# Performance work log

Measured on AMD Instinct MI355X. Metric: run time of the kernel, lower is better.

## Reference

```python
import jax, jax.numpy as jnp
import numpy as np

QW, KW = 64, 128          # atom query / key window sizes
PAD = (KW - QW) // 2      # halo on each side of the key window
DEPTH, HEADS = 3, 4

def ln(x):
    m = jnp.mean(x, -1, keepdims=True)
    v = jnp.var(x, -1, keepdims=True)
    return (x - m) * jax.lax.rsqrt(v + 1e-5)

def q_windows(x):
    # x: (B, N, ...) -> (B, n, QW, ...); N assumed multiple of QW
    B, N = x.shape[0], x.shape[1]
    n = N // QW
    return x.reshape((B, n, QW) + x.shape[2:])

def k_windows(x):
    # x: (B, N, ...) -> (B, n, KW, ...) sliding key windows with zero halo padding
    B, N = x.shape[0], x.shape[1]
    n = N // QW
    pad_cfg = [(0, 0), (PAD, n * QW + PAD - N)] + [(0, 0)] * (x.ndim - 2)
    xp = jnp.pad(x, pad_cfg)
    idx = jnp.arange(n)[:, None] * QW + jnp.arange(KW)[None, :]
    return xp[:, idx]


def setup_inputs() -> dict:
    key = jax.random.key(0)
    ks = jax.random.split(key, 24)
    B, N, DS, DP, DT, NT = 2, 8192, 128, 16, 384, 1024
    w = lambda k, shp: (jax.random.normal(k, shp, jnp.float32) / np.sqrt(shp[-2])).astype(jnp.float32)
    inp = {
        'ref_pos': jax.random.normal(ks[0], (B, N, 3), jnp.float32),
        'ref_charge': jax.random.normal(ks[1], (B, N, 1), jnp.float32),
        'ref_mask': jnp.ones((B, N, 1), jnp.float32),
        'ref_element': jax.random.uniform(ks[2], (B, N, 128), jnp.float32),
        'ref_atom_name_chars': jax.random.uniform(ks[3], (B, N, 256), jnp.float32),
        'W_single': w(ks[4], (389, DS)),
        'W_pair': w(ks[5], (5, DP)),
        'W_outer': w(ks[6], (DS, 2 * DP)),
        'Wp_ff1': w(ks[7], (DP, 4 * DP)),
        'Wp_ff2': w(ks[8], (4 * DP, DP)),
        'Wq': w(ks[9], (DEPTH, DS, DS)),
        'Wk': w(ks[10], (DEPTH, DS, DS)),
        'Wv': w(ks[11], (DEPTH, DS, DS)),
        'Wo': w(ks[12], (DEPTH, DS, DS)),
        'Wb': w(ks[13], (DP, HEADS)),
        'Wff1': w(ks[14], (DEPTH, DS, 4 * DS)),
        'Wff2': w(ks[15], (DEPTH, 4 * DS, DS)),
        'W_out': w(ks[16], (DS, DT)),
        'ref_space_uid': jnp.sort(jax.random.randint(ks[17], (B, N), 0, NT), axis=-1),
        'atom_to_token_idx': jnp.sort(jax.random.randint(ks[18], (B, N), 0, NT), axis=-1),
        'n_tokens': NT,
    }
    return inp


def reference(ref_pos, ref_charge, ref_mask, ref_element, ref_atom_name_chars,
              W_single, W_pair, W_outer, Wp_ff1, Wp_ff2,
              Wq, Wk, Wv, Wo, Wb, Wff1, Wff2, W_out,
              ref_space_uid, atom_to_token_idx, n_tokens):
    B, N, _ = ref_pos.shape
    n = N // QW
    feats = jnp.concatenate([ref_pos, ref_charge, ref_mask, ref_element, ref_atom_name_chars], -1)
    s = feats @ W_single                                    # (B,N,DS) atom single repr

    # windowed pairwise geometric features
    pos_i, pos_j = q_windows(ref_pos), k_windows(ref_pos)   # (B,n,QW,3), (B,n,KW,3)
    uid_i, uid_j = q_windows(ref_space_uid), k_windows(ref_space_uid)
    dij = pos_i[:, :, :, None, :] - pos_j[:, :, None, :, :]  # (B,n,QW,KW,3)
    inv = 1.0 / (1.0 + jnp.sum(dij * dij, -1, keepdims=True))
    bij = (uid_i[:, :, :, None] == uid_j[:, :, None, :])
    pf = jnp.concatenate([dij, inv, bij[..., None].astype(dij.dtype)], -1)  # (...,5)
    pair = (pf @ W_pair) * bij[..., None].astype(dij.dtype)  # (B,n,QW,KW,DP)

    # pairwise outer-add from relu(single): Linear(DS->2*DP) split into i/j halves
    p = jax.nn.relu(s) @ W_outer
    DP = pair.shape[-1]
    pi, pj = p[..., :DP], p[..., DP:]
    pair = pair + q_windows(pi)[:, :, :, None, :] + k_windows(pj)[:, :, None, :, :]
    pair = pair + jax.nn.relu(ln(pair) @ Wp_ff1) @ Wp_ff2    # pair FF (residual)
    bias = jnp.einsum('bnqkc,ch->bnhqk', pair, Wb)           # attn pair bias

    # key validity mask for the halo-padded positions
    kidx = jnp.arange(n)[:, None] * QW + jnp.arange(KW)[None, :] - PAD
    kmask = jnp.where((kidx >= 0) & (kidx < N), 0.0, -1e9).astype(s.dtype)  # (n,KW)

    dh = s.shape[-1] // HEADS
    x = s
    for l in range(DEPTH):
        h = ln(x)
        q = q_windows(h @ Wq[l]).reshape(B, n, QW, HEADS, dh)
        k = k_windows(h @ Wk[l]).reshape(B, n, KW, HEADS, dh)
        v = k_windows(h @ Wv[l]).reshape(B, n, KW, HEADS, dh)
        logits = jnp.einsum('bnqhd,bnkhd->bnhqk', q, k) / np.sqrt(dh)
        logits = logits + bias + kmask[None, :, None, None, :]
        a = jax.nn.softmax(logits, -1)
        o = jnp.einsum('bnhqk,bnkhd->bnqhd', a, v).reshape(B, N, -1) @ Wo[l]
        x = x + o
        x = x + jax.nn.relu(ln(x) @ Wff1[l]) @ Wff2[l]

    tok = jax.nn.relu(x @ W_out)                             # (B,N,DT)

    def seg_mean(src, idx_):
        ssum = jax.ops.segment_sum(src, idx_, num_segments=n_tokens)
        cnt = jax.ops.segment_sum(jnp.ones((src.shape[0],), src.dtype), idx_, num_segments=n_tokens)
        return ssum / jnp.clip(cnt, 1.0)[:, None]

    return jax.vmap(seg_mean)(tok, atom_to_token_idx)        # (B, n_tokens, DT)
```

## Files before the change

### kernel.cpp

```cpp
#include <hip/hip_runtime.h>
#include <hip/hip_bf16.h>

#define QW 64
#define KW 128
#define PADW 32
#define DEPTH 3
#define HEADS 4
#define B_ 2
#define N_ 8192
#define DS 128
#define DP 16
#define DT 384
#define NT 1024
#define NWIN (N_ / QW)
#define DH (DS / HEADS)

typedef unsigned short u16;
typedef __attribute__((ext_vector_type(8))) short short8;
typedef __attribute__((ext_vector_type(4))) float f32x4v;
typedef __attribute__((ext_vector_type(4))) unsigned short us4;

__device__ __forceinline__ u16 f2b(float x) {
    union { float f; unsigned u; } v; v.f = x;
    unsigned r = v.u + 0x7fffu + ((v.u >> 16) & 1u);
    return (u16)(r >> 16);
}
__device__ __forceinline__ float b2f(u16 h) {
    union { unsigned u; float f; } v; v.u = ((unsigned)h) << 16; return v.f;
}
__device__ __forceinline__ unsigned f2b2(float a, float b) {
    __hip_bfloat162 h = __float22bfloat162_rn(make_float2(a, b));
    union { __hip_bfloat162 h; unsigned u; } c; c.h = h; return c.u;
}
__device__ __forceinline__ us4 pack4(float a, float b, float c, float d) {
    union { us4 v; unsigned u[2]; } o;
    o.u[0] = f2b2(a, b);
    o.u[1] = f2b2(c, d);
    return o.v;
}

__global__ __launch_bounds__(256) void convw_kernel(
    const float* __restrict__ Wq, const float* __restrict__ Wk,
    const float* __restrict__ Wv, const float* __restrict__ Wo,
    const float* __restrict__ Wff1, const float* __restrict__ Wff2,
    const float* __restrict__ Wout, const float* __restrict__ Wpff1,
    const float* __restrict__ Wpff2, const float* __restrict__ Wb,
    const float* __restrict__ Wsingle, const float* __restrict__ Wouter,
    u16* __restrict__ qkvT, u16* __restrict__ woT, u16* __restrict__ ff1T,
    u16* __restrict__ ff2T, u16* __restrict__ woutT,
    u16* __restrict__ w1T32, u16* __restrict__ wcatT,
    u16* __restrict__ wsT, u16* __restrict__ woutrT)
{
    int idx = blockIdx.x * 256 + threadIdx.x;
    if (idx < 3 * 384 * 128) {
        int l = idx / (384 * 128), r = idx % (384 * 128);
        int n = r / 128, k = r % 128;
        const float* W = (n < 128) ? Wq : (n < 256) ? Wk : Wv;
        qkvT[idx] = f2b(W[(size_t)l * 16384 + k * 128 + (n & 127)]);
    }
    if (idx < 3 * 128 * 128) {
        int l = idx / 16384, r = idx % 16384;
        int n = r / 128, k = r % 128;
        woT[idx] = f2b(Wo[(size_t)l * 16384 + k * 128 + n]);
    }
    if (idx < 3 * 512 * 128) {
        int l = idx / 65536, r = idx % 65536;
        int n = r / 128, k = r % 128;
        ff1T[idx] = f2b(Wff1[(size_t)l * 65536 + k * 512 + n]);
    }
    if (idx < 3 * 128 * 512) {
        int l = idx / 65536, r = idx % 65536;
        int n = r / 512, k = r % 512;
        ff2T[idx] = f2b(Wff2[(size_t)l * 65536 + k * 128 + n]);
    }
    if (idx < 384 * 128) {
        int n = idx / 128, k = idx % 128;
        woutT[idx] = f2b(Wout[(size_t)k * 384 + n]);
    }
    if (idx < 64 * 32) {
        int n = idx >> 5, k = idx & 31;
        w1T32[idx] = (k < 16) ? f2b(Wpff1[k * 64 + n]) : (u16)0;
    }
    if (idx < 16 * 96) {
        int h = idx / 96, k = idx % 96;
        float s = 0.f;
        if (h < 4) {
            if (k < 16) s = Wb[k * 4 + h];
            else if (k < 80) {
                int j = k - 16;
                for (int c = 0; c < 16; ++c) s += Wpff2[j * 16 + c] * Wb[c * 4 + h];
            }
        }
        wcatT[idx] = f2b(s);
    }
    if (idx < 128 * 416) {
        int n = idx / 416, k = idx % 416;
        float v = 0.f;
        if (k < 128)       v = Wsingle[(5 + k) * 128 + n];
        else if (k < 384)  v = Wsingle[(133 + k - 128) * 128 + n];
        else if (k < 387)  v = Wsingle[(k - 384) * 128 + n];
        else if (k == 387) v = Wsingle[3 * 128 + n];
        else if (k == 388) v = Wsingle[4 * 128 + n];
        wsT[idx] = f2b(v);
    }
    if (idx < 32 * 128) {
        int n = idx >> 7, k = idx & 127;
        woutrT[idx] = f2b(Wouter[k * 32 + n]);
    }
}

__global__ __launch_bounds__(256) void embed_gemm(
    const float* __restrict__ pos, const float* __restrict__ charge,
    const float* __restrict__ mask, const float* __restrict__ elem,
    const float* __restrict__ chars, const u16* __restrict__ wsT,
    const u16* __restrict__ woutrT,
    float* __restrict__ X, u16* __restrict__ LNb, float* __restrict__ P)
{
    __shared__ __align__(16) u16 As[64 * 424];
    __shared__ float redS[64][4];
    int tid = threadIdx.x;
    int row0 = blockIdx.x * 64;

    #pragma unroll
    for (int it = 0; it < 8; ++it) {
        int idx = tid + it * 256;
        int r = idx >> 5, c4 = idx & 31;
        f32x4v v = *(const f32x4v*)(elem + (size_t)(row0 + r) * 128 + c4 * 4);
        *(us4*)&As[r * 424 + c4 * 4] = pack4(v[0], v[1], v[2], v[3]);
    }
    #pragma unroll
    for (int it = 0; it < 16; ++it) {
        int idx = tid + it * 256;
        int r = idx >> 6, c4 = idx & 63;
        f32x4v v = *(const f32x4v*)(chars + (size_t)(row0 + r) * 256 + c4 * 4);
        *(us4*)&As[r * 424 + 128 + c4 * 4] = pack4(v[0], v[1], v[2], v[3]);
    }
    if (tid < 64) {
        int g = row0 + tid;
        As[tid * 424 + 384] = f2b(pos[g * 3]);
        As[tid * 424 + 385] = f2b(pos[g * 3 + 1]);
        As[tid * 424 + 386] = f2b(pos[g * 3 + 2]);
        As[tid * 424 + 387] = f2b(charge[g]);
        As[tid * 424 + 388] = f2b(mask[g]);
        for (int c = 389; c < 416; ++c) As[tid * 424 + c] = 0;
    }
    __syncthreads();

    int wv = tid >> 6, lane = tid & 63, quad = lane >> 4, l16 = lane & 15;
    int wm = (wv & 1) * 32, wn = (wv >> 1) * 64;
    f32x4v acc[2][4];
    #pragma unroll
    for (int i = 0; i < 2; ++i)
        #pragma unroll
        for (int j = 0; j < 4; ++j) acc[i][j] = (f32x4v){0.f, 0.f, 0.f, 0.f};

    #pragma unroll
    for (int kk = 0; kk < 13; ++kk) {
        short8 a0 = *(short8*)&As[(wm + l16) * 424 + kk * 32 + quad * 8];
        short8 a1 = *(short8*)&As[(wm + 16 + l16) * 424 + kk * 32 + quad * 8];
        #pragma unroll
        for (int nt = 0; nt < 4; ++nt) {
            short8 bw = *(const short8*)&wsT[(size_t)(wn + nt * 16 + l16) * 416 +
                                             kk * 32 + quad * 8];
            acc[0][nt] = __builtin_amdgcn_mfma_f32_16x16x32_bf16(a0, bw, acc[0][nt], 0, 0, 0);
            acc[1][nt] = __builtin_amdgcn_mfma_f32_16x16x32_bf16(a1, bw, acc[1][nt], 0, 0, 0);
        }
    }
    __syncthreads();

    #pragma unroll
    for (int mt = 0; mt < 2; ++mt) {
        #pragma unroll
        for (int r = 0; r < 4; ++r) {
            int lrow = wm + mt * 16 + quad * 4 + r;
            int row = row0 + lrow;
            float s = 0.f, ss = 0.f;
            #pragma unroll
            for (int nt = 0; nt < 4; ++nt) {
                float v = acc[mt][nt][r];
                int col = wn + nt * 16 + l16;
                X[(size_t)row * DS + col] = v;
                As[lrow * 136 + col] = f2b(fmaxf(v, 0.f));
                s += v; ss += v * v;
            }
            #pragma unroll
            for (int o = 1; o < 16; o <<= 1) {
                s  += __shfl_xor(s, o);
                ss += __shfl_xor(ss, o);
            }
            if (l16 == 0) {
                redS[lrow][(wv >> 1) * 2]     = s;
                redS[lrow][(wv >> 1) * 2 + 1] = ss;
            }
        }
    }
    __syncthreads();

    #pragma unroll
    for (int mt = 0; mt < 2; ++mt)
        #pragma unroll
        for (int r = 0; r < 4; ++r) {
            int lrow = wm + mt * 16 + quad * 4 + r;
            int row = row0 + lrow;
            f32x4v rv = *(f32x4v*)&redS[lrow][0];
            float s = rv[0] + rv[2], ss = rv[1] + rv[3];
            float m = s * (1.f / 128.f);
            float var = ss * (1.f / 128.f) - m * m;
            float rs = rsqrtf(var + 1e-5f);
            #pragma unroll
            for (int nt = 0; nt < 4; ++nt) {
                int col = wn + nt * 16 + l16;
                LNb[(size_t)row * DS + col] = f2b((acc[mt][nt][r] - m) * rs);
            }
        }

    {
        f32x4v pacc[2];
        pacc[0] = (f32x4v){0.f, 0.f, 0.f, 0.f};
        pacc[1] = (f32x4v){0.f, 0.f, 0.f, 0.f};
        #pragma unroll
        for (int ks = 0; ks < 4; ++ks) {
            short8 a = *(short8*)&As[(wv * 16 + l16) * 136 + ks * 32 + quad * 8];
            #pragma unroll
            for (int nt = 0; nt < 2; ++nt) {
                short8 bw = *(const short8*)&woutrT[(size_t)(nt * 16 + l16) * 128 +
                                                    ks * 32 + quad * 8];
                pacc[nt] = __builtin_amdgcn_mfma_f32_16x16x32_bf16(a, bw, pacc[nt], 0, 0, 0);
            }
        }
        #pragma unroll
        for (int nt = 0; nt < 2; ++nt)
            #pragma unroll
            for (int r = 0; r < 4; ++r) {
                int row = row0 + wv * 16 + quad * 4 + r;
                P[(size_t)row * 32 + nt * 16 + l16] = pacc[nt][r];
            }
    }
}

__global__ __launch_bounds__(256) void bias_kernel(
    const float* __restrict__ pos, const int* __restrict__ uid,
    const float* __restrict__ P, const float* __restrict__ Wpair,
    const u16* __restrict__ w1T32, const u16* __restrict__ wcatT,
    u16* __restrict__ BIASb)
{
    __shared__ __align__(16) float posjS[128][4];
    __shared__ __align__(16) u16 lpS[4][16 * 24];
    __shared__ __align__(16) u16 A2S[4][16 * 104];

    int tid = threadIdx.x;
    int b  = blockIdx.x >> 11;
    int w  = (blockIdx.x >> 4) & 127;
    int qg = blockIdx.x & 15;

    if (tid < 128) {
        int r = tid;
        int jk = w * QW + r - PADW;
        bool valid = (jk >= 0) && (jk < N_);
        int gk = b * N_ + jk;
        float x = 0.f, y = 0.f, zz = 0.f; int u = 0;
        if (valid) { x = pos[gk * 3]; y = pos[gk * 3 + 1]; zz = pos[gk * 3 + 2]; u = uid[gk]; }
        posjS[r][0] = x; posjS[r][1] = y; posjS[r][2] = zz;
        ((int*)posjS[r])[3] = u;
    }

    int wv = tid >> 6, lane = tid & 63, quad = lane >> 4, l16 = lane & 15;
    int cl = lane >> 2, cg = lane & 3;
    int q = qg * 4 + wv;
    int gq = b * N_ + w * QW + q;

    float xi = pos[gq * 3], yi = pos[gq * 3 + 1], zi = pos[gq * 3 + 2];
    int ui = uid[gq];
    f32x4v pi4 = *(const f32x4v*)(P + (size_t)gq * 32 + cg * 4);
    f32x4v wp[5];
    #pragma unroll
    for (int f = 0; f < 5; ++f)
        wp[f] = *(const f32x4v*)(Wpair + f * 16 + cg * 4);
    short8 w1f[4], wcat[3];
    #pragma unroll
    for (int nt = 0; nt < 4; ++nt)
        w1f[nt] = *(const short8*)&w1T32[(nt * 16 + l16) * 32 + quad * 8];
    #pragma unroll
    for (int ks = 0; ks < 3; ++ks)
        wcat[ks] = *(const short8*)&wcatT[l16 * 96 + ks * 32 + quad * 8];

    f32x4v pjv[8];
    #pragma unroll
    for (int t = 0; t < 8; ++t) {
        int jk = w * QW + t * 16 + cl - PADW;
        bool valid = (jk >= 0) && (jk < N_);
        int gk = b * N_ + jk;
        f32x4v v = (f32x4v){0.f, 0.f, 0.f, 0.f};
        if (valid) v = *(const f32x4v*)(P + (size_t)gk * 32 + 16 + cg * 4);
        pjv[t] = v;
    }

    *(us4*)&A2S[wv][l16 * 104 + 80 + quad * 4] = (us4){0, 0, 0, 0};
    __syncthreads();

    size_t bbase = ((size_t)(b * NWIN + w) * HEADS) * (QW * KW);
    const short8 zero8 = (short8){0, 0, 0, 0, 0, 0, 0, 0};

    for (int t = 0; t < 8; ++t) {
        int kk1 = t * 16 + cl;
        float xj = posjS[kk1][0], yj = posjS[kk1][1], zj = posjS[kk1][2];
        int uj = ((int*)posjS[kk1])[3];
        float dx = xi - xj, dy = yi - yj, dz = zi - zj;
        float inv = 1.f / (1.f + dx * dx + dy * dy + dz * dz);
        float bf = (ui == uj) ? 1.f : 0.f;
        float pr[4];
        #pragma unroll
        for (int j = 0; j < 4; ++j) {
            float s = fmaf(dx, wp[0][j], fmaf(dy, wp[1][j],
                      fmaf(dz, wp[2][j], fmaf(inv, wp[3][j], wp[4][j]))));
            pr[j] = fmaf(bf, s, pi4[j] + pjv[t][j]);
        }
        float sum = pr[0] + pr[1] + pr[2] + pr[3];
        sum += __shfl_xor(sum, 1); sum += __shfl_xor(sum, 2);
        float m = sum * (1.f / 16.f);
        float d0 = pr[0] - m, d1 = pr[1] - m, d2 = pr[2] - m, d3 = pr[3] - m;
        float vs = d0 * d0 + d1 * d1 + d2 * d2 + d3 * d3;
        vs += __shfl_xor(vs, 1); vs += __shfl_xor(vs, 2);
        float rstd = rsqrtf(vs * (1.f / 16.f) + 1e-5f);
        *(us4*)&lpS[wv][cl * 24 + cg * 4] =
            pack4(d0 * rstd, d1 * rstd, d2 * rstd, d3 * rstd);
        *(us4*)&A2S[wv][cl * 104 + cg * 4] = pack4(pr[0], pr[1], pr[2], pr[3]);

        short8 blp = zero8;
        if (quad < 2) blp = *(short8*)&lpS[wv][l16 * 24 + quad * 8];
        #pragma unroll
        for (int nt = 0; nt < 4; ++nt) {
            f32x4v z4 = (f32x4v){0.f, 0.f, 0.f, 0.f};
            z4 = __builtin_amdgcn_mfma_f32_16x16x32_bf16(w1f[nt], blp, z4, 0, 0, 0);
            *(us4*)&A2S[wv][l16 * 104 + 16 + nt * 16 + quad * 4] =
                pack4(fmaxf(z4[0], 0.f), fmaxf(z4[1], 0.f),
                      fmaxf(z4[2], 0.f), fmaxf(z4[3], 0.f));
        }
        f32x4v acc = (f32x4v){0.f, 0.f, 0.f, 0.f};
        #pragma unroll
        for (int ks = 0; ks < 3; ++ks) {
            short8 a2 = *(short8*)&A2S[wv][l16 * 104 + ks * 32 + quad * 8];
            acc = __builtin_amdgcn_mfma_f32_16x16x32_bf16(a2, wcat[ks], acc, 0, 0, 0);
        }
        if (l16 < 4) {
            *(us4*)&BIASb[bbase + (size_t)l16 * (QW * KW) + q * KW +
                          t * 16 + quad * 4] = pack4(acc[0], acc[1], acc[2], acc[3]);
        }
    }
}

template <bool RELU>
__global__ __launch_bounds__(256) void gemm_bf(
    const u16* __restrict__ A, const u16* __restrict__ WT,
    u16* __restrict__ OutB, int N)
{
    __shared__ __align__(16) u16 As[64 * 136];
    int tid = threadIdx.x;
    int row0 = blockIdx.x * 64, n0 = blockIdx.y * 128;

    #pragma unroll
    for (int it = 0; it < 4; ++it) {
        int idx = tid + it * 256;
        int r = idx >> 4, c8 = idx & 15;
        *(short8*)&As[r * 136 + c8 * 8] =
            *(const short8*)&A[(size_t)(row0 + r) * 128 + c8 * 8];
    }
    __syncthreads();

    int wv = tid >> 6, lane = tid & 63, quad = lane >> 4, l16 = lane & 15;
    int wm = (wv & 1) * 32, wn = (wv >> 1) * 64;
    f32x4v acc[2][4];
    #pragma unroll
    for (int i = 0; i < 2; ++i)
        #pragma unroll
        for (int j = 0; j < 4; ++j) acc[i][j] = (f32x4v){0.f, 0.f, 0.f, 0.f};

    #pragma unroll
    for (int kk = 0; kk < 4; ++kk) {
        short8 a0 = *(short8*)&As[(wm + l16) * 136 + kk * 32 + quad * 8];
        short8 a1 = *(short8*)&As[(wm + 16 + l16) * 136 + kk * 32 + quad * 8];
        #pragma unroll
        for (int nt = 0; nt < 4; ++nt) {
            short8 bw = *(const short8*)&WT[(size_t)(n0 + wn + nt * 16 + l16) * 128 +
                                            kk * 32 + quad * 8];
            acc[0][nt] = __builtin_amdgcn_mfma_f32_16x16x32_bf16(a0, bw, acc[0][nt], 0, 0, 0);
            acc[1][nt] = __builtin_amdgcn_mfma_f32_16x16x32_bf16(a1, bw, acc[1][nt], 0, 0, 0);
        }
    }
    #pragma unroll
    for (int mt = 0; mt < 2; ++mt)
        #pragma unroll
        for (int nt = 0; nt < 4; ++nt)
            #pragma unroll
            for (int r = 0; r < 4; ++r) {
                int row = row0 + wm + mt * 16 + quad * 4 + r;
                int col = n0 + wn + nt * 16 + l16;
                float v = acc[mt][nt][r];
                if (RELU) v = fmaxf(v, 0.f);
                OutB[(size_t)row * N + col] = f2b(v);
            }
}

__global__ __launch_bounds__(256) void wo_ff_fused(
    const u16* __restrict__ Ob, const u16* __restrict__ woT,
    const u16* __restrict__ w1T, const u16* __restrict__ w2T,
    float* __restrict__ X, u16* __restrict__ LNb)
{
    __shared__ __align__(16) u16 As[32 * 136];
    __shared__ __align__(16) u16 Hs[32 * 520];
    __shared__ float redS[32][4];
    int tid = threadIdx.x;
    int row0 = blockIdx.x * 32;
    int wv = tid >> 6, lane = tid & 63, quad = lane >> 4, l16 = lane & 15;
    int wm = (wv & 1) * 16, wn = (wv >> 1) * 64;

    #pragma unroll
    for (int it = 0; it < 2; ++it) {
        int idx = tid + it * 256;
        int r = idx >> 4, c8 = idx & 15;
        *(short8*)&As[r * 136 + c8 * 8] =
            *(const short8*)&Ob[(size_t)(row0 + r) * 128 + c8 * 8];
    }
    __syncthreads();

    f32x4v acc[4];
    #pragma unroll
    for (int j = 0; j < 4; ++j) acc[j] = (f32x4v){0.f, 0.f, 0.f, 0.f};
    #pragma unroll
    for (int ks = 0; ks < 4; ++ks) {
        short8 a = *(short8*)&As[(wm + l16) * 136 + ks * 32 + quad * 8];
        #pragma unroll
        for (int nt = 0; nt < 4; ++nt) {
            short8 b = *(const short8*)&woT[(size_t)(wn + nt * 16 + l16) * 128 +
                                            ks * 32 + quad * 8];
            acc[nt] = __builtin_amdgcn_mfma_f32_16x16x32_bf16(a, b, acc[nt], 0, 0, 0);
        }
    }
    __syncthreads();

    #pragma unroll
    for (int r = 0; r < 4; ++r) {
        int lrow = wm + quad * 4 + r;
        int row = row0 + lrow;
        float s = 0.f, ss = 0.f;
        #pragma unroll
        for (int nt = 0; nt < 4; ++nt) {
            int col = wn + nt * 16 + l16;
            float v = acc[nt][r] + X[(size_t)row * DS + col];
            acc[nt][r] = v;
            s += v; ss += v * v;
        }
        #pragma unroll
        for (int o2 = 1; o2 < 16; o2 <<= 1) {
            s  += __shfl_xor(s, o2);
            ss += __shfl_xor(ss, o2);
        }
        if (l16 == 0) {
            redS[lrow][(wv >> 1) * 2]     = s;
            redS[lrow][(wv >> 1) * 2 + 1] = ss;
        }
    }
    __syncthreads();

    #pragma unroll
    for (int r = 0; r < 4; ++r) {
        int lrow = wm + quad * 4 + r;
        f32x4v rv = *(f32x4v*)&redS[lrow][0];
        float s = rv[0] + rv[2], ss = rv[1] + rv[3];
        float m = s * (1.f / 128.f);
        float var = ss * (1.f / 128.f) - m * m;
        float rs = rsqrtf(var + 1e-5f);
        #pragma unroll
        for (int nt = 0; nt < 4; ++nt) {
            int col = wn + nt * 16 + l16;
            As[lrow * 136 + col] = f2b((acc[nt][r] - m) * rs);
        }
    }
    __syncthreads();

    {
        short8 brow[2][4];
        #pragma unroll
        for (int nt = 0; nt < 2; ++nt)
            #pragma unroll
            for (int ks = 0; ks < 4; ++ks)
                brow[nt][ks] = *(short8*)&As[(nt * 16 + l16) * 136 + ks * 32 + quad * 8];
        #pragma unroll
        for (int mt = 0; mt < 8; ++mt) {
            int j0 = wv * 128 + mt * 16;
            f32x4v c0 = (f32x4v){0.f, 0.f, 0.f, 0.f};
            f32x4v c1 = (f32x4v){0.f, 0.f, 0.f, 0.f};
            #pragma unroll
            for (int ks = 0; ks < 4; ++ks) {
                short8 aw = *(const short8*)&w1T[(size_t)(j0 + l16) * 128 +
                                                 ks * 32 + quad * 8];
                c0 = __builtin_amdgcn_mfma_f32_16x16x32_bf16(aw, brow[0][ks], c0, 0, 0, 0);
                c1 = __builtin_amdgcn_mfma_f32_16x16x32_bf16(aw, brow[1][ks], c1, 0, 0, 0);
            }
            *(us4*)&Hs[l16 * 520 + j0 + quad * 4] =
                pack4(fmaxf(c0[0], 0.f), fmaxf(c0[1], 0.f),
                      fmaxf(c0[2], 0.f), fmaxf(c0[3], 0.f));
            *(us4*)&Hs[(16 + l16) * 520 + j0 + quad * 4] =
                pack4(fmaxf(c1[0], 0.f), fmaxf(c1[1], 0.f),
                      fmaxf(c1[2], 0.f), fmaxf(c1[3], 0.f));
        }
    }
    __syncthreads();

    f32x4v acc2[4];
    #pragma unroll
    for (int j = 0; j < 4; ++j) acc2[j] = (f32x4v){0.f, 0.f, 0.f, 0.f};
    #pragma unroll
    for (int ks = 0; ks < 16; ++ks) {
        short8 a = *(short8*)&Hs[(wm + l16) * 520 + ks * 32 + quad * 8];
        #pragma unroll
        for (int nt = 0; nt < 4; ++nt) {
            short8 b = *(const short8*)&w2T[(size_t)(wn + nt * 16 + l16) * 512 +
                                            ks * 32 + quad * 8];
            acc2[nt] = __builtin_amdgcn_mfma_f32_16x16x32_bf16(a, b, acc2[nt], 0, 0, 0);
        }
    }

    #pragma unroll
    for (int r = 0; r < 4; ++r) {
        int lrow = wm + quad * 4 + r;
        int row = row0 + lrow;
        float s = 0.f, ss = 0.f;
        #pragma unroll
        for (int nt = 0; nt < 4; ++nt) {
            int col = wn + nt * 16 + l16;
            float v = acc2[nt][r] + acc[nt][r];
            acc2[nt][r] = v;
            X[(size_t)row * DS + col] = v;
            s += v; ss += v * v;
        }
        #pragma unroll
        for (int o2 = 1; o2 < 16; o2 <<= 1) {
            s  += __shfl_xor(s, o2);
            ss += __shfl_xor(ss, o2);
        }
        if (l16 == 0) {
            redS[lrow][(wv >> 1) * 2]     = s;
            redS[lrow][(wv >> 1) * 2 + 1] = ss;
        }
    }
    __syncthreads();

    #pragma unroll
    for (int r = 0; r < 4; ++r) {
        int lrow = wm + quad * 4 + r;
        int row = row0 + lrow;
        f32x4v rv = *(f32x4v*)&redS[lrow][0];
        float s = rv[0] + rv[2], ss = rv[1] + rv[3];
        float m = s * (1.f / 128.f);
        float var = ss * (1.f / 128.f) - m * m;
        float rs = rsqrtf(var + 1e-5f);
        #pragma unroll
        for (int nt = 0; nt < 4; ++nt) {
            int col = wn + nt * 16 + l16;
            LNb[(size_t)row * DS + col] = f2b((acc2[nt][r] - m) * rs);
        }
    }
}

__global__ __launch_bounds__(256) void gemm_fin(
    const float* __restrict__ A, const u16* __restrict__ WT,
    u16* __restrict__ OutB, int K, int N)
{
    __shared__ __align__(16) u16 As[64 * 88];
    const int row0 = blockIdx.x * 64, n0 = blockIdx.y * 128;
    const int tid = threadIdx.x;
    const int w = tid >> 6, lane = tid & 63, quad = lane >> 4, l16 = lane & 15;
    const int wm = (w & 1) * 32, wn = (w >> 1) * 64;

    f32x4v acc[2][4];
    #pragma unroll
    for (int i = 0; i < 2; ++i)
        #pragma unroll
        for (int j = 0; j < 4; ++j) acc[i][j] = (f32x4v){0.f, 0.f, 0.f, 0.f};

    for (int k0 = 0; k0 < K; k0 += 64) {
        __syncthreads();
        #pragma unroll
        for (int it = 0; it < 4; ++it) {
            int idx = tid + it * 256;
            int r = idx >> 4, c = idx & 15;
            f32x4v v = *(const f32x4v*)(A + (size_t)(row0 + r) * K + k0 + c * 4);
            *(us4*)&As[r * 88 + c * 4] = pack4(v[0], v[1], v[2], v[3]);
        }
        __syncthreads();
        #pragma unroll
        for (int kk = 0; kk < 64; kk += 32) {
            short8 a0 = *(const short8*)&As[(wm + l16) * 88 + kk + quad * 8];
            short8 a1 = *(const short8*)&As[(wm + 16 + l16) * 88 + kk + quad * 8];
            #pragma unroll
            for (int nt = 0; nt < 4; ++nt) {
                short8 b = *(const short8*)&WT[(size_t)(n0 + wn + nt * 16 + l16) * K + k0 + kk + quad * 8];
                acc[0][nt] = __builtin_amdgcn_mfma_f32_16x16x32_bf16(a0, b, acc[0][nt], 0, 0, 0);
                acc[1][nt] = __builtin_amdgcn_mfma_f32_16x16x32_bf16(a1, b, acc[1][nt], 0, 0, 0);
            }
        }
    }
    #pragma unroll
    for (int mt = 0; mt < 2; ++mt)
        #pragma unroll
        for (int nt = 0; nt < 4; ++nt)
            #pragma unroll
            for (int r = 0; r < 4; ++r) {
                int row = row0 + wm + mt * 16 + quad * 4 + r;
                int col = n0 + wn + nt * 16 + l16;
                OutB[(size_t)row * N + col] = f2b(fmaxf(acc[mt][nt][r], 0.f));
            }
}

__global__ __launch_bounds__(256) void attn_kernel(
    const u16* __restrict__ QKV, const u16* __restrict__ BIASb,
    u16* __restrict__ O)
{
    __shared__ __align__(16) u16 sQ[64 * 40];
    __shared__ __align__(16) u16 sK[128 * 40];
    __shared__ __align__(16) u16 sVt[32 * 152];
    __shared__ __align__(16) u16 sP[64 * 136];
    __shared__ float pmax[4][64];
    __shared__ float psum[4][64];
    __shared__ float gfac[4][64];

    int tid = threadIdx.x;
    int h = blockIdx.x & 3, w = (blockIdx.x >> 2) & 127, b = blockIdx.x >> 9;
    size_t rowbase = (size_t)b * N_ + w * QW;
    size_t bbase = ((size_t)(b * NWIN + w) * HEADS + h) * (QW * KW);
    const short8 zero8 = (short8){0, 0, 0, 0, 0, 0, 0, 0};

    {
        int r = tid >> 2, d8 = (tid & 3) * 8;
        *(short8*)&sQ[r * 40 + d8] =
            *(const short8*)&QKV[(rowbase + r) * 384 + h * DH + d8];
    }
    #pragma unroll
    for (int i = 0; i < 2; ++i) {
        int idx = tid + i * 256;
        int r = idx >> 2, d8 = (idx & 3) * 8;
        int jk = w * QW + r - PADW;
        short8 v = zero8;
        if (jk >= 0 && jk < N_)
            v = *(const short8*)&QKV[((size_t)b * N_ + jk) * 384 + 128 + h * DH + d8];
        *(short8*)&sK[r * 40 + d8] = v;
    }
    {
        int kk = tid >> 1, d0 = (tid & 1) * 16;
        int jk = w * QW + kk - PADW;
        short8 v0 = zero8, v1 = zero8;
        if (jk >= 0 && jk < N_) {
            const u16* src = &QKV[((size_t)b * N_ + jk) * 384 + 256 + h * DH + d0];
            v0 = *(const short8*)src;
            v1 = *(const short8*)(src + 8);
        }
        #pragma unroll
        for (int j = 0; j < 8; ++j) {
            sVt[(d0 + j) * 152 + kk] = (u16)v0[j];
            sVt[(d0 + 8 + j) * 152 + kk] = (u16)v1[j];
        }
    }
    #pragma unroll
    for (int i = 0; i < 4; ++i) {
        int idx = tid + i * 256;
        int q = idx >> 4, c8 = idx & 15;
        *(short8*)&sP[q * 136 + c8 * 8] =
            *(const short8*)&BIASb[bbase + (size_t)q * KW + c8 * 8];
    }
    __syncthreads();

    int wv = tid >> 6, lane = tid & 63, quad = lane >> 4, l16 = lane & 15;
    const float scale = 0.17677669529663687f;

    short8 aq[4];
    #pragma unroll
    for (int mt = 0; mt < 4; ++mt)
        aq[mt] = *(short8*)&sQ[(mt * 16 + l16) * 40 + quad * 8];
    float e[2][4][4];
    #pragma unroll
    for (int ni = 0; ni < 2; ++ni) {
        int nt = wv * 2 + ni;
        short8 bk = *(short8*)&sK[(nt * 16 + l16) * 40 + quad * 8];
        int kk = nt * 16 + l16;
        int jk = w * QW + kk - PADW;
        float msk = (jk >= 0 && jk < N_) ? 0.f : -1e9f;
        #pragma unroll
        for (int mt = 0; mt < 4; ++mt) {
            f32x4v acc = (f32x4v){0.f, 0.f, 0.f, 0.f};
            acc = __builtin_amdgcn_mfma_f32_16x16x32_bf16(aq[mt], bk, acc, 0, 0, 0);
            #pragma unroll
            for (int r = 0; r < 4; ++r) {
                int q = mt * 16 + quad * 4 + r;
                e[ni][mt][r] = acc[r] * scale + b2f(sP[q * 136 + kk]) + msk;
            }
        }
    }

    #pragma unroll
    for (int mt = 0; mt < 4; ++mt)
        #pragma unroll
        for (int r = 0; r < 4; ++r) {
            float m = fmaxf(e[0][mt][r], e[1][mt][r]);
            m = fmaxf(m, __shfl_xor(m, 1));
            m = fmaxf(m, __shfl_xor(m, 2));
            m = fmaxf(m, __shfl_xor(m, 4));
            m = fmaxf(m, __shfl_xor(m, 8));
            float e0 = __expf(e[0][mt][r] - m);
            float e1 = __expf(e[1][mt][r] - m);
            e[0][mt][r] = e0; e[1][mt][r] = e1;
            float s = e0 + e1;
            s += __shfl_xor(s, 1);
            s += __shfl_xor(s, 2);
            s += __shfl_xor(s, 4);
            s += __shfl_xor(s, 8);
            if (l16 == 0) {
                int q = mt * 16 + quad * 4 + r;
                pmax[wv][q] = m;
                psum[wv][q] = s;
            }
        }
    __syncthreads();

    if (tid < 64) {
        float m0 = pmax[0][tid], m1 = pmax[1][tid], m2 = pmax[2][tid], m3 = pmax[3][tid];
        float M = fmaxf(fmaxf(m0, m1), fmaxf(m2, m3));
        float g0 = __expf(m0 - M), g1 = __expf(m1 - M),
              g2 = __expf(m2 - M), g3 = __expf(m3 - M);
        float T = psum[0][tid] * g0 + psum[1][tid] * g1 +
                  psum[2][tid] * g2 + psum[3][tid] * g3;
        float inv = 1.f / T;
        gfac[0][tid] = g0 * inv; gfac[1][tid] = g1 * inv;
        gfac[2][tid] = g2 * inv; gfac[3][tid] = g3 * inv;
    }
    __syncthreads();

    #pragma unroll
    for (int mt = 0; mt < 4; ++mt)
        #pragma unroll
        for (int r = 0; r < 4; ++r) {
            int q = mt * 16 + quad * 4 + r;
            float f = gfac[wv][q];
            #pragma unroll
            for (int ni = 0; ni < 2; ++ni) {
                int kk = (wv * 2 + ni) * 16 + l16;
                sP[q * 136 + kk] = f2b(e[ni][mt][r] * f);
            }
        }
    __syncthreads();

    {
        int mt = wv;
        short8 ap[4];
        #pragma unroll
        for (int ks = 0; ks < 4; ++ks)
            ap[ks] = *(short8*)&sP[(mt * 16 + l16) * 136 + ks * 32 + quad * 8];
        #pragma unroll
        for (int nt = 0; nt < 2; ++nt) {
            f32x4v acc = (f32x4v){0.f, 0.f, 0.f, 0.f};
            #pragma unroll
            for (int ks = 0; ks < 4; ++ks) {
                short8 bv = *(short8*)&sVt[(nt * 16 + l16) * 152 + ks * 32 + quad * 8];
                acc = __builtin_amdgcn_mfma_f32_16x16x32_bf16(ap[ks], bv, acc, 0, 0, 0);
            }
            int d = nt * 16 + l16;
            #pragma unroll
            for (int r = 0; r < 4; ++r) {
                int q = mt * 16 + quad * 4 + r;
                O[(rowbase + q) * DS + h * DH + d] = f2b(acc[r]);
            }
        }
    }
}

__global__ __launch_bounds__(128) void seg_kernel(
    const u16* __restrict__ TOKb, const int* __restrict__ idx,
    float* __restrict__ out)
{
    int t = blockIdx.x & (NT - 1);
    int b = blockIdx.x >> 10;
    const int* id = idx + (size_t)b * N_;

    int lo = 0, hi = N_;
    while (lo < hi) { int mid = (lo + hi) >> 1; if (id[mid] < t) lo = mid + 1; else hi = mid; }
    int start = lo;
    hi = N_;
    while (lo < hi) { int mid = (lo + hi) >> 1; if (id[mid] < t + 1) lo = mid + 1; else hi = mid; }
    int end = lo;

    float inv = 1.f / fmaxf((float)(end - start), 1.f);
    for (int c = threadIdx.x; c < DT; c += 128) {
        float s = 0.f;
        for (int r = start; r < end; ++r) s += b2f(TOKb[((size_t)b * N_ + r) * DT + c]);
        out[((size_t)b * NT + t) * DT + c] = s * inv;
    }
}

extern "C" void kernel_launch(void* const* d_in, const int* in_sizes, int n_in,
                              void* d_out, int out_size, void* d_ws, size_t ws_size,
                              hipStream_t stream)
{
    const float* ref_pos    = (const float*)d_in[0];
    const float* ref_charge = (const float*)d_in[1];
    const float* ref_mask   = (const float*)d_in[2];
    const float* ref_elem   = (const float*)d_in[3];
    const float* ref_chars  = (const float*)d_in[4];
    const float* W_single   = (const float*)d_in[5];
    const float* W_pair     = (const float*)d_in[6];
    const float* W_outer    = (const float*)d_in[7];
    const float* Wp_ff1     = (const float*)d_in[8];
    const float* Wp_ff2     = (const float*)d_in[9];
    const float* Wq         = (const float*)d_in[10];
    const float* Wk         = (const float*)d_in[11];
    const float* Wv         = (const float*)d_in[12];
    const float* Wo         = (const float*)d_in[13];
    const float* Wb         = (const float*)d_in[14];
    const float* Wff1       = (const float*)d_in[15];
    const float* Wff2       = (const float*)d_in[16];
    const float* W_out      = (const float*)d_in[17];
    const int*   uid        = (const int*)d_in[18];
    const int*   a2t        = (const int*)d_in[19];
    float* out = (float*)d_out;

    const size_t ROWS = (size_t)B_ * N_;
    float* ws = (float*)d_ws;
    float* X    = ws;
    float* P    = X + ROWS * DS;
    u16* QKVb   = (u16*)(P + ROWS * 32);
    u16* Ob     = QKVb + ROWS * 384;
    u16* FFb    = Ob + ROWS * DS;
    u16* BIASb  = FFb + ROWS * 512;
    u16* TOKb   = BIASb + (size_t)B_ * NWIN * HEADS * QW * KW;
    u16* LNb    = TOKb + ROWS * DT;
    u16* qkvT   = LNb + ROWS * DS;
    u16* woT    = qkvT + 3 * 384 * 128;
    u16* ff1T   = woT + 3 * 128 * 128;
    u16* ff2T   = ff1T + 3 * 512 * 128;
    u16* woutT  = ff2T + 3 * 128 * 512;
    u16* w1T32  = woutT + 384 * 128;
    u16* wcatT  = w1T32 + 64 * 32;
    u16* wsT    = wcatT + 16 * 96;
    u16* woutrT = wsT + 128 * 416;

    convw_kernel<<<768, 256, 0, stream>>>(Wq, Wk, Wv, Wo, Wff1, Wff2, W_out,
                                          Wp_ff1, Wp_ff2, Wb, W_single, W_outer,
                                          qkvT, woT, ff1T, ff2T, woutT,
                                          w1T32, wcatT, wsT, woutrT);
    embed_gemm<<<ROWS / 64, 256, 0, stream>>>(ref_pos, ref_charge, ref_mask,
                                              ref_elem, ref_chars, wsT, woutrT,
                                              X, LNb, P);
    bias_kernel<<<4096, 256, 0, stream>>>(ref_pos, uid, P, W_pair,
                                          w1T32, wcatT, BIASb);

    for (int l = 0; l < DEPTH; ++l) {
        gemm_bf<false><<<dim3(ROWS / 64, 3), 256, 0, stream>>>(
            LNb, qkvT + (size_t)l * 384 * 128, QKVb, 384);
        attn_kernel<<<B_ * NWIN * HEADS, 256, 0, stream>>>(QKVb, BIASb, Ob);
        wo_ff_fused<<<ROWS / 32, 256, 0, stream>>>(
            Ob, woT + (size_t)l * 128 * 128,
            ff1T + (size_t)l * 512 * 128, ff2T + (size_t)l * 128 * 512,
            X, LNb);
    }

    gemm_fin<<<dim3(ROWS / 64, 3), 256, 0, stream>>>(X, woutT, TOKb, DS, DT);
    seg_kernel<<<B_ * NT, 128, 0, stream>>>(TOKb, a2t, out);
}
```

Before: 405.6 us.

## Fuse QKV projection and output projection into preceding kernels' epilogues

The QKV projection GEMM moves into the epilogue of embed_gemm (layer 0) and wo_ff_fused (layers 1..2). The LayerNorm output stays in shared memory instead of round-tripping through global LNb. The final W_out GEMM with ReLU is likewise fused into the last wo_ff_fused, which removes four separate GEMM launches and the LNb/X reloads. In exchange, each fused block now reads all three 128-column weight chunks, and wo_ff_fused does a serial 32x384 GEMM per block, which lengthens those kernels.

New measurement: 405.1 us. About the same (-0.1%).

```diff
diff --git a/kernel.cpp b/kernel.cpp
--- a/kernel.cpp
+++ b/kernel.cpp
@@ -113,11 +113,12 @@
     const float* __restrict__ pos, const float* __restrict__ charge,
     const float* __restrict__ mask, const float* __restrict__ elem,
     const float* __restrict__ chars, const u16* __restrict__ wsT,
-    const u16* __restrict__ woutrT,
-    float* __restrict__ X, u16* __restrict__ LNb, float* __restrict__ P)
+    const u16* __restrict__ woutrT, const u16* __restrict__ qkv0T,
+    float* __restrict__ X, float* __restrict__ P, u16* __restrict__ QKVb)
 {
     __shared__ __align__(16) u16 As[64 * 424];
     __shared__ float redS[64][4];
+    const int LNOFF = 64 * 136;
     int tid = threadIdx.x;
     int row0 = blockIdx.x * 64;
 
@@ -201,7 +202,6 @@
         #pragma unroll
         for (int r = 0; r < 4; ++r) {
             int lrow = wm + mt * 16 + quad * 4 + r;
-            int row = row0 + lrow;
             f32x4v rv = *(f32x4v*)&redS[lrow][0];
             float s = rv[0] + rv[2], ss = rv[1] + rv[3];
             float m = s * (1.f / 128.f);
@@ -210,7 +210,7 @@
             #pragma unroll
             for (int nt = 0; nt < 4; ++nt) {
                 int col = wn + nt * 16 + l16;
-                LNb[(size_t)row * DS + col] = f2b((acc[mt][nt][r] - m) * rs);
+                As[LNOFF + lrow * 136 + col] = f2b((acc[mt][nt][r] - m) * rs);
             }
         }
 
@@ -235,6 +235,38 @@
                 int row = row0 + wv * 16 + quad * 4 + r;
                 P[(size_t)row * 32 + nt * 16 + l16] = pacc[nt][r];
             }
+    }
+    __syncthreads();
+
+    for (int c = 0; c < 3; ++c) {
+        int n0c = c * 128;
+        f32x4v qa[2][4];
+        #pragma unroll
+        for (int i = 0; i < 2; ++i)
+            #pragma unroll
+            for (int j = 0; j < 4; ++j) qa[i][j] = (f32x4v){0.f, 0.f, 0.f, 0.f};
+        #pragma unroll
+        for (int ks = 0; ks < 4; ++ks) {
+            short8 a0 = *(short8*)&As[LNOFF + (wm + l16) * 136 + ks * 32 + quad * 8];
+            short8 a1 = *(short8*)&As[LNOFF + (wm + 16 + l16) * 136 + ks * 32 + quad * 8];
+            #pragma unroll
+            for (int nt = 0; nt < 4; ++nt) {
+                short8 bw = *(const short8*)&qkv0T[(size_t)(n0c + wn + nt * 16 + l16) * 128 +
+                                                   ks * 32 + quad * 8];
+                qa[0][nt] = __builtin_amdgcn_mfma_f32_16x16x32_bf16(a0, bw, qa[0][nt], 0, 0, 0);
+                qa[1][nt] = __builtin_amdgcn_mfma_f32_16x16x32_bf16(a1, bw, qa[1][nt], 0, 0, 0);
+            }
+        }
+        #pragma unroll
+        for (int mt = 0; mt < 2; ++mt)
+            #pragma unroll
+            for (int nt = 0; nt < 4; ++nt)
+                #pragma unroll
+                for (int r = 0; r < 4; ++r) {
+                    int row = row0 + wm + mt * 16 + quad * 4 + r;
+                    int col = n0c + wn + nt * 16 + l16;
+                    QKVb[(size_t)row * 384 + col] = f2b(qa[mt][nt][r]);
+                }
     }
 }
 
@@ -349,62 +381,12 @@
     }
 }
 
-template <bool RELU>
-__global__ __launch_bounds__(256) void gemm_bf(
-    const u16* __restrict__ A, const u16* __restrict__ WT,
-    u16* __restrict__ OutB, int N)
-{
-    __shared__ __align__(16) u16 As[64 * 136];
-    int tid = threadIdx.x;
-    int row0 = blockIdx.x * 64, n0 = blockIdx.y * 128;
-
-    #pragma unroll
-    for (int it = 0; it < 4; ++it) {
-        int idx = tid + it * 256;
-        int r = idx >> 4, c8 = idx & 15;
-        *(short8*)&As[r * 136 + c8 * 8] =
-            *(const short8*)&A[(size_t)(row0 + r) * 128 + c8 * 8];
-    }
-    __syncthreads();
-
-    int wv = tid >> 6, lane = tid & 63, quad = lane >> 4, l16 = lane & 15;
-    int wm = (wv & 1) * 32, wn = (wv >> 1) * 64;
-    f32x4v acc[2][4];
-    #pragma unroll
-    for (int i = 0; i < 2; ++i)
-        #pragma unroll
-        for (int j = 0; j < 4; ++j) acc[i][j] = (f32x4v){0.f, 0.f, 0.f, 0.f};
-
-    #pragma unroll
-    for (int kk = 0; kk < 4; ++kk) {
-        short8 a0 = *(short8*)&As[(wm + l16) * 136 + kk * 32 + quad * 8];
-        short8 a1 = *(short8*)&As[(wm + 16 + l16) * 136 + kk * 32 + quad * 8];
-        #pragma unroll
-        for (int nt = 0; nt < 4; ++nt) {
-            short8 bw = *(const short8*)&WT[(size_t)(n0 + wn + nt * 16 + l16) * 128 +
-                                            kk * 32 + quad * 8];
-            acc[0][nt] = __builtin_amdgcn_mfma_f32_16x16x32_bf16(a0, bw, acc[0][nt], 0, 0, 0);
-            acc[1][nt] = __builtin_amdgcn_mfma_f32_16x16x32_bf16(a1, bw, acc[1][nt], 0, 0, 0);
-        }
-    }
-    #pragma unroll
-    for (int mt = 0; mt < 2; ++mt)
-        #pragma unroll
-        for (int nt = 0; nt < 4; ++nt)
-            #pragma unroll
-            for (int r = 0; r < 4; ++r) {
-                int row = row0 + wm + mt * 16 + quad * 4 + r;
-                int col = n0 + wn + nt * 16 + l16;
-                float v = acc[mt][nt][r];
-                if (RELU) v = fmaxf(v, 0.f);
-                OutB[(size_t)row * N + col] = f2b(v);
-            }
-}
-
+template <bool LAST>
 __global__ __launch_bounds__(256) void wo_ff_fused(
     const u16* __restrict__ Ob, const u16* __restrict__ woT,
     const u16* __restrict__ w1T, const u16* __restrict__ w2T,
-    float* __restrict__ X, u16* __restrict__ LNb)
+    const u16* __restrict__ auxT, float* __restrict__ X,
+    u16* __restrict__ OutB)
 {
     __shared__ __align__(16) u16 As[32 * 136];
     __shared__ __align__(16) u16 Hs[32 * 520];
@@ -549,68 +531,49 @@
     #pragma unroll
     for (int r = 0; r < 4; ++r) {
         int lrow = wm + quad * 4 + r;
-        int row = row0 + lrow;
-        f32x4v rv = *(f32x4v*)&redS[lrow][0];
-        float s = rv[0] + rv[2], ss = rv[1] + rv[3];
-        float m = s * (1.f / 128.f);
-        float var = ss * (1.f / 128.f) - m * m;
-        float rs = rsqrtf(var + 1e-5f);
+        float m = 0.f, rs = 1.f;
+        if (!LAST) {
+            f32x4v rv = *(f32x4v*)&redS[lrow][0];
+            float s = rv[0] + rv[2], ss = rv[1] + rv[3];
+            m = s * (1.f / 128.f);
+            float var = ss * (1.f / 128.f) - m * m;
+            rs = rsqrtf(var + 1e-5f);
+        }
         #pragma unroll
         for (int nt = 0; nt < 4; ++nt) {
             int col = wn + nt * 16 + l16;
-            LNb[(size_t)row * DS + col] = f2b((acc2[nt][r] - m) * rs);
-        }
-    }
-}
-
-__global__ __launch_bounds__(256) void gemm_fin(
-    const float* __restrict__ A, const u16* __restrict__ WT,
-    u16* __restrict__ OutB, int K, int N)
-{
-    __shared__ __align__(16) u16 As[64 * 88];
-    const int row0 = blockIdx.x * 64, n0 = blockIdx.y * 128;
-    const int tid = threadIdx.x;
-    const int w = tid >> 6, lane = tid & 63, quad = lane >> 4, l16 = lane & 15;
-    const int wm = (w & 1) * 32, wn = (w >> 1) * 64;
-
-    f32x4v acc[2][4];
-    #pragma unroll
-    for (int i = 0; i < 2; ++i)
-        #pragma unroll
-        for (int j = 0; j < 4; ++j) acc[i][j] = (f32x4v){0.f, 0.f, 0.f, 0.f};
-
-    for (int k0 = 0; k0 < K; k0 += 64) {
-        __syncthreads();
-        #pragma unroll
-        for (int it = 0; it < 4; ++it) {
-            int idx = tid + it * 256;
-            int r = idx >> 4, c = idx & 15;
-            f32x4v v = *(const f32x4v*)(A + (size_t)(row0 + r) * K + k0 + c * 4);
-            *(us4*)&As[r * 88 + c * 4] = pack4(v[0], v[1], v[2], v[3]);
-        }
-        __syncthreads();
-        #pragma unroll
-        for (int kk = 0; kk < 64; kk += 32) {
-            short8 a0 = *(const short8*)&As[(wm + l16) * 88 + kk + quad * 8];
-            short8 a1 = *(const short8*)&As[(wm + 16 + l16) * 88 + kk + quad * 8];
+            float v = acc2[nt][r];
+            As[lrow * 136 + col] = f2b(LAST ? v : (v - m) * rs);
+        }
+    }
+    __syncthreads();
+
+    for (int c = 0; c < 3; ++c) {
+        int n0c = c * 128;
+        f32x4v qa[4];
+        #pragma unroll
+        for (int j = 0; j < 4; ++j) qa[j] = (f32x4v){0.f, 0.f, 0.f, 0.f};
+        #pragma unroll
+        for (int ks = 0; ks < 4; ++ks) {
+            short8 a = *(short8*)&As[(wm + l16) * 136 + ks * 32 + quad * 8];
             #pragma unroll
             for (int nt = 0; nt < 4; ++nt) {
-                short8 b = *(const short8*)&WT[(size_t)(n0 + wn + nt * 16 + l16) * K + k0 + kk + quad * 8];
-                acc[0][nt] = __builtin_amdgcn_mfma_f32_16x16x32_bf16(a0, b, acc[0][nt], 0, 0, 0);
-                acc[1][nt] = __builtin_amdgcn_mfma_f32_16x16x32_bf16(a1, b, acc[1][nt], 0, 0, 0);
-            }
-        }
-    }
-    #pragma unroll
-    for (int mt = 0; mt < 2; ++mt)
+                short8 b = *(const short8*)&auxT[(size_t)(n0c + wn + nt * 16 + l16) * 128 +
+                                                 ks * 32 + quad * 8];
+                qa[nt] = __builtin_amdgcn_mfma_f32_16x16x32_bf16(a, b, qa[nt], 0, 0, 0);
+            }
+        }
         #pragma unroll
         for (int nt = 0; nt < 4; ++nt)
             #pragma unroll
             for (int r = 0; r < 4; ++r) {
-                int row = row0 + wm + mt * 16 + quad * 4 + r;
-                int col = n0 + wn + nt * 16 + l16;
-                OutB[(size_t)row * N + col] = f2b(fmaxf(acc[mt][nt][r], 0.f));
-            }
+                int row = row0 + wm + quad * 4 + r;
+                int col = n0c + wn + nt * 16 + l16;
+                float v = qa[nt][r];
+                if (LAST) v = fmaxf(v, 0.f);
+                OutB[(size_t)row * 384 + col] = f2b(v);
+            }
+    }
 }
 
 __global__ __launch_bounds__(256) void attn_kernel(
@@ -848,20 +811,24 @@
                                           w1T32, wcatT, wsT, woutrT);
     embed_gemm<<<ROWS / 64, 256, 0, stream>>>(ref_pos, ref_charge, ref_mask,
                                               ref_elem, ref_chars, wsT, woutrT,
-                                              X, LNb, P);
+                                              qkvT, X, P, QKVb);
     bias_kernel<<<4096, 256, 0, stream>>>(ref_pos, uid, P, W_pair,
                                           w1T32, wcatT, BIASb);
 
     for (int l = 0; l < DEPTH; ++l) {
-        gemm_bf<false><<<dim3(ROWS / 64, 3), 256, 0, stream>>>(
-            LNb, qkvT + (size_t)l * 384 * 128, QKVb, 384);
         attn_kernel<<<B_ * NWIN * HEADS, 256, 0, stream>>>(QKVb, BIASb, Ob);
-        wo_ff_fused<<<ROWS / 32, 256, 0, stream>>>(
-            Ob, woT + (size_t)l * 128 * 128,
-            ff1T + (size_t)l * 512 * 128, ff2T + (size_t)l * 128 * 512,
-            X, LNb);
-    }
-
-    gemm_fin<<<dim3(ROWS / 64, 3), 256, 0, stream>>>(X, woutT, TOKb, DS, DT);
+        if (l < DEPTH - 1) {
+            wo_ff_fused<false><<<ROWS / 32, 256, 0, stream>>>(
+                Ob, woT + (size_t)l * 128 * 128,
+                ff1T + (size_t)l * 512 * 128, ff2T + (size_t)l * 128 * 512,
+                qkvT + (size_t)(l + 1) * 384 * 128, X, QKVb);
+        } else {
+            wo_ff_fused<true><<<ROWS / 32, 256, 0, stream>>>(
+                Ob, woT + (size_t)l * 128 * 128,
+                ff1T + (size_t)l * 512 * 128, ff2T + (size_t)l * 128 * 512,
+                woutT, X, TOKb);
+        }
+    }
+
     seg_kernel<<<B_ * NT, 128, 0, stream>>>(TOKb, a2t, out);
 }
```
